# Optimization experiments

Measured on AMD Instinct MI355X. Metric: run time of the kernel, lower is better.

Reference implementation:

```python
import jax, jax.numpy as jnp
import numpy as np

D_MODEL = 1024
NHEAD = 16
HEAD_DIM = D_MODEL // NHEAD
DFF = 4096
EPS = 1e-5


def _layernorm(x, g, b):
    mu = jnp.mean(x, axis=-1, keepdims=True)
    var = jnp.mean(jnp.square(x - mu), axis=-1, keepdims=True)
    return (x - mu) * jax.lax.rsqrt(var + EPS) * g + b


def setup_inputs() -> dict:
    key = jax.random.key(0)
    ks = jax.random.split(key, 20)
    B, S = 2, 2048
    s = 0.02
    inp = {
        "src": jax.random.normal(ks[0], (B, S, D_MODEL), jnp.float32),
        "recompute_idx": jnp.sort(jax.random.randint(ks[1], (409,), 0, S)),
        "cached_k": jax.random.normal(ks[2], (B, NHEAD, S, HEAD_DIM), jnp.float32),
        "cached_v": jax.random.normal(ks[3], (B, NHEAD, S, HEAD_DIM), jnp.float32),
        "Wq": jax.random.normal(ks[4], (D_MODEL, D_MODEL), jnp.float32) * s,
        "bq": jnp.zeros((D_MODEL,), jnp.float32),
        "Wk": jax.random.normal(ks[5], (D_MODEL, D_MODEL), jnp.float32) * s,
        "bk": jnp.zeros((D_MODEL,), jnp.float32),
        "Wv": jax.random.normal(ks[6], (D_MODEL, D_MODEL), jnp.float32) * s,
        "bv": jnp.zeros((D_MODEL,), jnp.float32),
        "Wo": jax.random.normal(ks[7], (D_MODEL, D_MODEL), jnp.float32) * s,
        "bo": jnp.zeros((D_MODEL,), jnp.float32),
        "W1": jax.random.normal(ks[8], (DFF, D_MODEL), jnp.float32) * s,
        "b1": jnp.zeros((DFF,), jnp.float32),
        "W2": jax.random.normal(ks[9], (D_MODEL, DFF), jnp.float32) * s,
        "b2": jnp.zeros((D_MODEL,), jnp.float32),
        "g1": jnp.ones((D_MODEL,), jnp.float32),
        "beta1": jnp.zeros((D_MODEL,), jnp.float32),
        "g2": jnp.ones((D_MODEL,), jnp.float32),
        "beta2": jnp.zeros((D_MODEL,), jnp.float32),
    }
    return inp


def reference(src, recompute_idx, cached_k, cached_v, Wq, bq, Wk, bk, Wv, bv,
              Wo, bo, W1, b1, W2, b2, g1, beta1, g2, beta2):
    B, S, D = src.shape
    H, hd = NHEAD, HEAD_DIM

    # Q for all tokens
    q = (src @ Wq.T + bq).reshape(B, S, H, hd).transpose(0, 2, 1, 3)  # [B,H,S,hd]

    # K/V recomputed only for selected tokens, scattered over cached KV
    src_rec = src[:, recompute_idx, :]  # [B,R,D]
    R = src_rec.shape[1]
    k_rec = (src_rec @ Wk.T + bk).reshape(B, R, H, hd).transpose(0, 2, 1, 3)
    v_rec = (src_rec @ Wv.T + bv).reshape(B, R, H, hd).transpose(0, 2, 1, 3)
    k_full = cached_k.at[:, :, recompute_idx, :].set(k_rec)  # [B,H,S,hd]
    v_full = cached_v.at[:, :, recompute_idx, :].set(v_rec)

    # attention over mixed cached/fresh KV
    scores = jnp.einsum('bhqd,bhkd->bhqk', q, k_full) / np.sqrt(hd).astype(src.dtype)
    probs = jax.nn.softmax(scores, axis=-1)
    attn = jnp.einsum('bhqk,bhkd->bhqd', probs, v_full)
    attn = attn.transpose(0, 2, 1, 3).reshape(B, S, D)
    attn = attn @ Wo.T + bo

    x = _layernorm(src + attn, g1, beta1)
    ff = jax.nn.relu(x @ W1.T + b1) @ W2.T + b2
    x = _layernorm(x + ff, g2, beta2)
    return x
```

## Files before the change

### kernel.cpp

```cpp
#include <hip/hip_runtime.h>
#include <hip/hip_bf16.h>

typedef __attribute__((ext_vector_type(4))) float f32x4;
typedef __attribute__((ext_vector_type(8))) short s16x8;
typedef __attribute__((ext_vector_type(4))) short s16x4;
typedef __attribute__((ext_vector_type(2))) short s16x2;

typedef __attribute__((address_space(1))) const unsigned int guint;
typedef __attribute__((address_space(3))) unsigned int luint;

#define D_MODEL 1024
#define NHEAD 16
#define HEAD_DIM 64
#define DFF 4096
#define SEQ 2048
#define BATCH 2

__device__ __forceinline__ float b2f(short s) {
  union { unsigned int u; float f; } v;
  v.u = ((unsigned int)(unsigned short)s) << 16;
  return v.f;
}
__device__ __forceinline__ short f2b(float f) {
  __hip_bfloat16 h = __float2bfloat16(f);
  return *reinterpret_cast<short*>(&h);
}
__device__ __forceinline__ s16x8 cvt8(f32x4 a, f32x4 b) {
  s16x8 r;
  #pragma unroll
  for (int i = 0; i < 4; ++i) { r[i] = f2b(a[i]); r[i + 4] = f2b(b[i]); }
  return r;
}

template<int MODE, int BN, bool AF32, bool WF32>
__global__ __launch_bounds__(256, 3)
void gemm_nt(const void* __restrict__ Av, const void* __restrict__ Wv,
             const float* __restrict__ bias, short* __restrict__ out,
             int M, int N, int K,
             const int* __restrict__ idx, int R,
             const float* __restrict__ bias2, const float* __restrict__ bias3,
             short* __restrict__ pB, short* __restrict__ pC,
             short* __restrict__ pD)
{
  constexpr bool GLDS = (!AF32 && !WF32);
  constexpr int NI = BN / 32;

  const float* Af = (const float*)Av;
  const short* Ab = (const short*)Av;
  const float* Wf = (const float*)Wv;
  const short* Wb = (const short*)Wv;

  const int tid  = threadIdx.x;
  const int lane = tid & 63, wave = tid >> 6;
  const int g = lane >> 4, l15 = lane & 15;
  const int wm = (wave & 1) * 64, wn = (wave >> 1) * (BN / 2);

  const int nwg = gridDim.x * gridDim.y;
  int lid = blockIdx.y * gridDim.x + blockIdx.x;
  if ((nwg & 7) == 0) lid = (lid & 7) * (nwg >> 3) + (lid >> 3);
  const int bn = lid % gridDim.x;
  const int bm0 = lid / gridDim.x;

  int task = 0, bm = bm0, Mt = M;
  if (MODE == 8) {
    if (bm0 < 32)      { task = 0; bm = bm0;      Mt = M; }
    else if (bm0 < 39) { task = 1; bm = bm0 - 32; Mt = BATCH * R; }
    else               { task = 2; bm = bm0 - 39; Mt = BATCH * R; }
  }

  f32x4 acc[4][NI] = {};

  if constexpr (GLDS) {
    __shared__ short As[2][128][32];
    __shared__ short Bs[2][BN][32];

    const short* Wbase = Wb + ((MODE == 8) ? ((size_t)task << 20) : 0);
    const int nz   = (MODE == 6) ? gridDim.z : 1;
    const int Keff = K / nz;
    const int kOff = (MODE == 6) ? (int)blockIdx.z * Keff : 0;

    const int rA0 = wave * 16 + (lane >> 2);
    const int rA1 = rA0 + 64;
    const int c0  = (lane & 3) * 8;

    auto arow = [&](int r) -> long {
      const int gm = bm * 128 + r;
      const int am = gm < Mt ? gm : Mt - 1;
      if (MODE == 8 && task > 0) {
        const int b0 = am / R;
        return (long)(b0 * SEQ + idx[am - b0 * R]);
      }
      return am;
    };
    const long aR0 = arow(rA0), aR1 = arow(rA1);
    const long wR0 = (long)bn * BN + rA0;

    const short* gA0 = Ab + aR0 * K + kOff + c0;
    const short* gA1 = Ab + aR1 * K + kOff + c0;
    const short* gB0 = Wbase + wR0 * K + kOff + c0;
    const short* gB1 = nullptr;
    if constexpr (BN == 128) gB1 = Wbase + ((long)bn * BN + rA1) * K + kOff + c0;

    auto stage = [&](int buf, int k0) {
      luint* lA0 = (luint*)((short*)As + buf * 4096 + wave * 512);
      luint* lA1 = (luint*)((short*)As + buf * 4096 + (4 + wave) * 512);
      luint* lB0 = (luint*)((short*)Bs + buf * (BN * 32) + wave * 512);
      __builtin_amdgcn_global_load_lds((guint*)(gA0 + k0), lA0, 16, 0, 0);
      __builtin_amdgcn_global_load_lds((guint*)(gA1 + k0), lA1, 16, 0, 0);
      __builtin_amdgcn_global_load_lds((guint*)(gB0 + k0), lB0, 16, 0, 0);
      if constexpr (BN == 128) {
        luint* lB1 = (luint*)((short*)Bs + buf * (BN * 32) + (4 + wave) * 512);
        __builtin_amdgcn_global_load_lds((guint*)(gB1 + k0), lB1, 16, 0, 0);
      }
    };

    stage(0, 0);
    __syncthreads();
    int cur = 0;
    for (int k0 = 0; k0 < Keff; k0 += 32) {
      const int k1 = k0 + 32;
      if (k1 < Keff) stage(cur ^ 1, k1);

      s16x8 af[4], bf4[NI];
      #pragma unroll
      for (int mi = 0; mi < 4; ++mi)
        af[mi] = *(const s16x8*)&As[cur][wm + mi * 16 + l15][g * 8];
      #pragma unroll
      for (int ni = 0; ni < NI; ++ni)
        bf4[ni] = *(const s16x8*)&Bs[cur][wn + ni * 16 + l15][g * 8];
      #pragma unroll
      for (int mi = 0; mi < 4; ++mi)
        #pragma unroll
        for (int ni = 0; ni < NI; ++ni)
          acc[mi][ni] = __builtin_amdgcn_mfma_f32_16x16x32_bf16(af[mi], bf4[ni], acc[mi][ni], 0, 0, 0);

      __syncthreads();
      cur ^= 1;
    }
  } else {
    __shared__ short As[128][40];
    __shared__ short Bs[128][40];
    const int r0 = tid >> 1, c0 = (tid & 1) * 16;
    const int gm0 = bm * 128 + r0;
    const int am0 = gm0 < M ? gm0 : M - 1;
    long aRow0;
    if (MODE == 3 || MODE == 4) {
      const int b0 = am0 / R;
      aRow0 = (long)(b0 * SEQ + idx[am0 - b0 * R]);
    } else {
      aRow0 = am0;
    }
    const long wRow0 = bn * 128 + r0;

    for (int k0 = 0; k0 < K; k0 += 32) {
      __syncthreads();
      if (AF32) {
        f32x4 a0 = *(const f32x4*)(Af + aRow0 * K + k0 + c0);
        f32x4 a1 = *(const f32x4*)(Af + aRow0 * K + k0 + c0 + 4);
        f32x4 a2 = *(const f32x4*)(Af + aRow0 * K + k0 + c0 + 8);
        f32x4 a3 = *(const f32x4*)(Af + aRow0 * K + k0 + c0 + 12);
        *(s16x8*)&As[r0][c0]     = cvt8(a0, a1);
        *(s16x8*)&As[r0][c0 + 8] = cvt8(a2, a3);
      } else {
        *(s16x8*)&As[r0][c0]     = *(const s16x8*)(Ab + aRow0 * K + k0 + c0);
        *(s16x8*)&As[r0][c0 + 8] = *(const s16x8*)(Ab + aRow0 * K + k0 + c0 + 8);
      }
      if (WF32) {
        f32x4 w0 = *(const f32x4*)(Wf + wRow0 * K + k0 + c0);
        f32x4 w1 = *(const f32x4*)(Wf + wRow0 * K + k0 + c0 + 4);
        f32x4 w2 = *(const f32x4*)(Wf + wRow0 * K + k0 + c0 + 8);
        f32x4 w3 = *(const f32x4*)(Wf + wRow0 * K + k0 + c0 + 12);
        *(s16x8*)&Bs[r0][c0]     = cvt8(w0, w1);
        *(s16x8*)&Bs[r0][c0 + 8] = cvt8(w2, w3);
      } else {
        *(s16x8*)&Bs[r0][c0]     = *(const s16x8*)(Wb + wRow0 * K + k0 + c0);
        *(s16x8*)&Bs[r0][c0 + 8] = *(const s16x8*)(Wb + wRow0 * K + k0 + c0 + 8);
      }
      __syncthreads();

      s16x8 af[4], bf4[4];
      #pragma unroll
      for (int mi = 0; mi < 4; ++mi)
        af[mi] = *(const s16x8*)&As[wm + mi * 16 + l15][g * 8];
      #pragma unroll
      for (int ni = 0; ni < 4; ++ni)
        bf4[ni] = *(const s16x8*)&Bs[wn + ni * 16 + l15][g * 8];
      #pragma unroll
      for (int mi = 0; mi < 4; ++mi)
        #pragma unroll
        for (int ni = 0; ni < 4; ++ni)
          acc[mi][ni % NI] = __builtin_amdgcn_mfma_f32_16x16x32_bf16(af[mi], bf4[ni], acc[mi][ni % NI], 0, 0, 0);
    }
  }

  short* outz = out;
  if (MODE == 6) {
    const int z = blockIdx.z;
    outz = (z == 0) ? out : (z == 1) ? pB : (z == 2) ? pC : pD;
  }

  #pragma unroll
  for (int mi = 0; mi < 4; ++mi) {
    #pragma unroll
    for (int ni = 0; ni < NI; ++ni) {
      const int gn = bn * BN + wn + ni * 16 + l15;
      float bv;
      if (MODE == 6)      bv = 0.f;
      else if (MODE == 8) bv = (task == 0) ? bias[gn] : (task == 1) ? bias2[gn] : bias3[gn];
      else                bv = bias[gn];
      #pragma unroll
      for (int r = 0; r < 4; ++r) {
        const int gm = bm * 128 + wm + mi * 16 + g * 4 + r;
        if (MODE == 8) { if (gm >= Mt) continue; }
        else           { if (gm >= M)  continue; }
        float v = acc[mi][ni][r] + bv;
        if (MODE == 1) v = v > 0.f ? v : 0.f;
        if (MODE == 2) v *= 0.125f;
        if (MODE == 0 || MODE == 1) {
          out[(long)gm * N + gn] = f2b(v);
        } else if (MODE == 2) {
          const int b = gm >> 11, s = gm & (SEQ - 1);
          const int h = gn >> 6, d = gn & 63;
          out[(((long)(b * NHEAD + h)) * SEQ + s) * 64 + d] = f2b(v);
        } else if (MODE == 3) {
          const int b = gm / R, s = idx[gm - b * R];
          const int h = gn >> 6, d = gn & 63;
          out[(((long)(b * NHEAD + h)) * SEQ + s) * 64 + d] = f2b(v);
        } else if (MODE == 4) {
          const int b = gm / R, s = idx[gm - b * R];
          const int h = gn >> 6, d = gn & 63;
          out[(((long)(b * NHEAD + h)) * 64 + d) * SEQ + s] = f2b(v);
        } else if (MODE == 6) {
          outz[(long)gm * N + gn] = f2b(v);
        } else {
          const int h = gn >> 6, d = gn & 63;
          if (task == 0) {
            const int b = gm >> 11, s = gm & (SEQ - 1);
            out[(((long)(b * NHEAD + h)) * SEQ + s) * 64 + d] = f2b(v * 0.125f);
          } else if (task == 1) {
            const int b = gm / R, s = idx[gm - b * R];
            (out + (1L << 22))[(((long)(b * NHEAD + h)) * SEQ + s) * 64 + d] = f2b(v);
          } else {
            const int b = gm / R, s = idx[gm - b * R];
            (out + (1L << 23))[(((long)(b * NHEAD + h)) * 64 + d) * SEQ + s] = f2b(v);
          }
        }
      }
    }
  }
}

__global__ __launch_bounds__(256, 2)
void attn_fwd(const short* __restrict__ Q, const short* __restrict__ Kf,
              const short* __restrict__ Vt, short* __restrict__ out)
{
  __shared__ short Kl[2][64][64];
  __shared__ short Vl[2][64][64];

  const int tid  = threadIdx.x;
  const int lane = tid & 63, w = tid >> 6;
  const int g = lane >> 4, l15 = lane & 15;
  const int bh = blockIdx.x;
  const int qt = blockIdx.y;
  const int b  = bh >> 4, h = bh & 15;

  const long base = (long)bh * SEQ * 64;
  const int  q0   = qt * 128 + w * 32;

  s16x8 qf[2][2];
  #pragma unroll
  for (int mi = 0; mi < 2; ++mi)
    #pragma unroll
    for (int c = 0; c < 2; ++c)
      qf[mi][c] = *(const s16x8*)(Q + base + (long)(q0 + mi * 16 + l15) * 64 + c * 32 + g * 8);

  float lsum[2] = {0.f, 0.f};
  f32x4 o[2][4] = {};

  auto ldsw = [](short (*buf)[64], int row, int slot) -> short* {
    return (short*)((char*)&buf[0][0] + row * 128 + ((slot ^ (row & 7)) << 4));
  };

  const int c20 = tid, c21 = tid + 256;
  const int r0 = c20 >> 3, s0 = c20 & 7;
  const int r1 = c21 >> 3, s1 = c21 & 7;

  s16x8 kr[2], vr[2];
  kr[0] = *(const s16x8*)(Kf + base + (long)r0 * 64 + s0 * 8);
  kr[1] = *(const s16x8*)(Kf + base + (long)r1 * 64 + s1 * 8);
  vr[0] = *(const s16x8*)(Vt + base + (long)r0 * SEQ + s0 * 8);
  vr[1] = *(const s16x8*)(Vt + base + (long)r1 * SEQ + s1 * 8);
  *(s16x8*)ldsw(Kl[0], r0, s0) = kr[0];
  *(s16x8*)ldsw(Kl[0], r1, s1) = kr[1];
  *(s16x8*)ldsw(Vl[0], r0, s0) = vr[0];
  *(s16x8*)ldsw(Vl[0], r1, s1) = vr[1];

  int cur = 0;
  for (int t = 0; t < SEQ / 64; ++t) {
    __syncthreads();
    const int kvn = (t + 1) * 64;
    if (kvn < SEQ) {
      kr[0] = *(const s16x8*)(Kf + base + (long)(kvn + r0) * 64 + s0 * 8);
      kr[1] = *(const s16x8*)(Kf + base + (long)(kvn + r1) * 64 + s1 * 8);
      vr[0] = *(const s16x8*)(Vt + base + (long)r0 * SEQ + kvn + s0 * 8);
      vr[1] = *(const s16x8*)(Vt + base + (long)r1 * SEQ + kvn + s1 * 8);
    }

    f32x4 sc[2][4] = {};
    __builtin_amdgcn_s_setprio(1);
    #pragma unroll
    for (int c = 0; c < 2; ++c)
      #pragma unroll
      for (int n = 0; n < 4; ++n) {
        s16x8 kb = *(const s16x8*)ldsw(Kl[cur], n * 16 + l15, c * 4 + g);
        sc[0][n] = __builtin_amdgcn_mfma_f32_16x16x32_bf16(kb, qf[0][c], sc[0][n], 0, 0, 0);
        sc[1][n] = __builtin_amdgcn_mfma_f32_16x16x32_bf16(kb, qf[1][c], sc[1][n], 0, 0, 0);
      }
    __builtin_amdgcn_s_setprio(0);

    s16x8 pa[2][2];
    #pragma unroll
    for (int mi = 0; mi < 2; ++mi) {
      #pragma unroll
      for (int n = 0; n < 4; ++n)
        #pragma unroll
        for (int r = 0; r < 4; ++r) {
          sc[mi][n][r] = __expf(sc[mi][n][r]);
          lsum[mi] += sc[mi][n][r];
        }
      unsigned int wpk[4][2];
      #pragma unroll
      for (int n = 0; n < 4; ++n)
        #pragma unroll
        for (int p = 0; p < 2; ++p)
          asm("v_cvt_pk_bf16_f32 %0, %1, %2"
              : "=v"(wpk[n][p]) : "v"(sc[mi][n][2 * p]), "v"(sc[mi][n][2 * p + 1]));
      #pragma unroll
      for (int c = 0; c < 2; ++c) {
        union { s16x8 v; unsigned int u[4]; } pu;
        #pragma unroll
        for (int p = 0; p < 2; ++p) {
          unsigned int a = wpk[2 * c][p], bb = wpk[2 * c + 1][p];
          asm volatile("v_permlane32_swap_b32 %0, %1" : "+v"(a), "+v"(bb));
          asm volatile("v_permlane16_swap_b32 %0, %1" : "+v"(a), "+v"(bb));
          pu.u[p]     = a;
          pu.u[2 + p] = bb;
        }
        pa[mi][c] = pu.v;
      }
    }

    __builtin_amdgcn_s_setprio(1);
    #pragma unroll
    for (int dt = 0; dt < 4; ++dt)
      #pragma unroll
      for (int c = 0; c < 2; ++c) {
        s16x8 vb = *(const s16x8*)ldsw(Vl[cur], dt * 16 + l15, c * 4 + g);
        o[0][dt] = __builtin_amdgcn_mfma_f32_16x16x32_bf16(pa[0][c], vb, o[0][dt], 0, 0, 0);
        o[1][dt] = __builtin_amdgcn_mfma_f32_16x16x32_bf16(pa[1][c], vb, o[1][dt], 0, 0, 0);
      }
    __builtin_amdgcn_s_setprio(0);

    if (kvn < SEQ) {
      *(s16x8*)ldsw(Kl[cur ^ 1], r0, s0) = kr[0];
      *(s16x8*)ldsw(Kl[cur ^ 1], r1, s1) = kr[1];
      *(s16x8*)ldsw(Vl[cur ^ 1], r0, s0) = vr[0];
      *(s16x8*)ldsw(Vl[cur ^ 1], r1, s1) = vr[1];
    }
    cur ^= 1;
  }

  float inv[2][4];
  #pragma unroll
  for (int mi = 0; mi < 2; ++mi) {
    float tt = lsum[mi];
    tt += __shfl_xor(tt, 16, 64);
    tt += __shfl_xor(tt, 32, 64);
    #pragma unroll
    for (int r = 0; r < 4; ++r)
      inv[mi][r] = 1.0f / __shfl(tt, g * 4 + r, 64);
  }

  #pragma unroll
  for (int mi = 0; mi < 2; ++mi)
    #pragma unroll
    for (int dt = 0; dt < 4; ++dt)
      #pragma unroll
      for (int r = 0; r < 4; ++r) {
        const int q   = q0 + mi * 16 + g * 4 + r;
        const int col = h * 64 + dt * 16 + l15;
        out[((long)(b * SEQ + q)) * D_MODEL + col] = f2b(o[mi][dt][r] * inv[mi][r]);
      }
}

template<bool RES_F32, bool OUT_F32>
__global__ __launch_bounds__(256, 4)
void ln_ff2(const short* __restrict__ p0, const short* __restrict__ p1,
            const float* __restrict__ bias, const void* __restrict__ resv,
            const float* __restrict__ g, const float* __restrict__ beta,
            void* __restrict__ outv)
{
  __shared__ float red[8];
  const int row = blockIdx.x;
  const int tid = threadIdx.x;
  const int lane = tid & 63, w = tid >> 6;

  s16x4 v0 = *(const s16x4*)(p0 + (long)row * D_MODEL + tid * 4);
  s16x4 v1 = *(const s16x4*)(p1 + (long)row * D_MODEL + tid * 4);
  f32x4 vb = *(const f32x4*)(bias + tid * 4);
  float x[4];
  if (RES_F32) {
    f32x4 vr = *(const f32x4*)((const float*)resv + (long)row * D_MODEL + tid * 4);
    #pragma unroll
    for (int i = 0; i < 4; ++i) x[i] = vr[i] + b2f(v0[i]) + b2f(v1[i]) + vb[i];
  } else {
    s16x4 vr = *(const s16x4*)((const short*)resv + (long)row * D_MODEL + tid * 4);
    #pragma unroll
    for (int i = 0; i < 4; ++i) x[i] = b2f(vr[i]) + b2f(v0[i]) + b2f(v1[i]) + vb[i];
  }

  float sum = x[0] + x[1] + x[2] + x[3];
  #pragma unroll
  for (int msk = 32; msk >= 1; msk >>= 1) sum += __shfl_xor(sum, msk, 64);
  if (lane == 0) red[w] = sum;
  __syncthreads();
  sum = red[0] + red[1] + red[2] + red[3];
  const float mu = sum * (1.f / D_MODEL);

  float sq = 0.f;
  #pragma unroll
  for (int i = 0; i < 4; ++i) { float d = x[i] - mu; sq += d * d; }
  #pragma unroll
  for (int msk = 32; msk >= 1; msk >>= 1) sq += __shfl_xor(sq, msk, 64);
  if (lane == 0) red[4 + w] = sq;
  __syncthreads();
  sq = red[4] + red[5] + red[6] + red[7];
  const float rs = rsqrtf(sq * (1.f / D_MODEL) + 1e-5f);

  if (OUT_F32) {
    f32x4 ov;
    #pragma unroll
    for (int i = 0; i < 4; ++i) {
      const int c = tid * 4 + i;
      ov[i] = (x[i] - mu) * rs * g[c] + beta[c];
    }
    *(f32x4*)((float*)outv + (long)row * D_MODEL + tid * 4) = ov;
  } else {
    s16x4 ov;
    #pragma unroll
    for (int i = 0; i < 4; ++i) {
      const int c = tid * 4 + i;
      ov[i] = f2b((x[i] - mu) * rs * g[c] + beta[c]);
    }
    *(s16x4*)((short*)outv + (long)row * D_MODEL + tid * 4) = ov;
  }
}

__global__ __launch_bounds__(256, 4)
void ln_ff4(const short* __restrict__ p0, const short* __restrict__ p1,
            const short* __restrict__ p2, const short* __restrict__ p3,
            const float* __restrict__ bias, const short* __restrict__ xres,
            const float* __restrict__ g, const float* __restrict__ beta,
            float* __restrict__ outv)
{
  __shared__ float red[8];
  const int row = blockIdx.x;
  const int tid = threadIdx.x;
  const int lane = tid & 63, w = tid >> 6;

  s16x4 v0 = *(const s16x4*)(p0 + (long)row * D_MODEL + tid * 4);
  s16x4 v1 = *(const s16x4*)(p1 + (long)row * D_MODEL + tid * 4);
  s16x4 v2 = *(const s16x4*)(p2 + (long)row * D_MODEL + tid * 4);
  s16x4 v3 = *(const s16x4*)(p3 + (long)row * D_MODEL + tid * 4);
  s16x4 vx = *(const s16x4*)(xres + (long)row * D_MODEL + tid * 4);
  f32x4 vb = *(const f32x4*)(bias + tid * 4);
  float x[4];
  #pragma unroll
  for (int i = 0; i < 4; ++i)
    x[i] = b2f(vx[i]) + b2f(v0[i]) + b2f(v1[i]) + b2f(v2[i]) + b2f(v3[i]) + vb[i];

  float sum = x[0] + x[1] + x[2] + x[3];
  #pragma unroll
  for (int msk = 32; msk >= 1; msk >>= 1) sum += __shfl_xor(sum, msk, 64);
  if (lane == 0) red[w] = sum;
  __syncthreads();
  sum = red[0] + red[1] + red[2] + red[3];
  const float mu = sum * (1.f / D_MODEL);

  float sq = 0.f;
  #pragma unroll
  for (int i = 0; i < 4; ++i) { float d = x[i] - mu; sq += d * d; }
  #pragma unroll
  for (int msk = 32; msk >= 1; msk >>= 1) sq += __shfl_xor(sq, msk, 64);
  if (lane == 0) red[4 + w] = sq;
  __syncthreads();
  sq = red[4] + red[5] + red[6] + red[7];
  const float rs = rsqrtf(sq * (1.f / D_MODEL) + 1e-5f);

  f32x4 ov;
  #pragma unroll
  for (int i = 0; i < 4; ++i) {
    const int c = tid * 4 + i;
    ov[i] = (x[i] - mu) * rs * g[c] + beta[c];
  }
  *(f32x4*)(outv + (long)row * D_MODEL + tid * 4) = ov;
}

template<bool RES_F32, bool OUT_F32>
__global__ __launch_bounds__(256, 4)
void ln_res(const short* __restrict__ a, const void* __restrict__ resv,
            const float* __restrict__ g, const float* __restrict__ beta,
            void* __restrict__ outv)
{
  __shared__ float red[8];
  const int row = blockIdx.x;
  const int tid = threadIdx.x;
  const int lane = tid & 63, w = tid >> 6;

  s16x4 va = *(const s16x4*)(a + (long)row * D_MODEL + tid * 4);
  float x[4];
  if (RES_F32) {
    f32x4 vr = *(const f32x4*)((const float*)resv + (long)row * D_MODEL + tid * 4);
    #pragma unroll
    for (int i = 0; i < 4; ++i) x[i] = b2f(va[i]) + vr[i];
  } else {
    s16x4 vr = *(const s16x4*)((const short*)resv + (long)row * D_MODEL + tid * 4);
    #pragma unroll
    for (int i = 0; i < 4; ++i) x[i] = b2f(va[i]) + b2f(vr[i]);
  }
  float sum = x[0] + x[1] + x[2] + x[3];
  #pragma unroll
  for (int msk = 32; msk >= 1; msk >>= 1) sum += __shfl_xor(sum, msk, 64);
  if (lane == 0) red[w] = sum;
  __syncthreads();
  sum = red[0] + red[1] + red[2] + red[3];
  const float mu = sum * (1.f / D_MODEL);

  float sq = 0.f;
  #pragma unroll
  for (int i = 0; i < 4; ++i) { float d = x[i] - mu; sq += d * d; }
  #pragma unroll
  for (int msk = 32; msk >= 1; msk >>= 1) sq += __shfl_xor(sq, msk, 64);
  if (lane == 0) red[4 + w] = sq;
  __syncthreads();
  sq = red[4] + red[5] + red[6] + red[7];
  const float rs = rsqrtf(sq * (1.f / D_MODEL) + 1e-5f);

  if (OUT_F32) {
    f32x4 ov;
    #pragma unroll
    for (int i = 0; i < 4; ++i) {
      const int c = tid * 4 + i;
      ov[i] = (x[i] - mu) * rs * g[c] + beta[c];
    }
    *(f32x4*)((float*)outv + (long)row * D_MODEL + tid * 4) = ov;
  } else {
    s16x4 ov;
    #pragma unroll
    for (int i = 0; i < 4; ++i) {
      const int c = tid * 4 + i;
      ov[i] = f2b((x[i] - mu) * rs * g[c] + beta[c]);
    }
    *(s16x4*)((short*)outv + (long)row * D_MODEL + tid * 4) = ov;
  }
}

__global__ void cvt_all(const float* __restrict__ ck, const float* __restrict__ cv,
                        const float* __restrict__ src,
                        const float* __restrict__ Wq, const float* __restrict__ Wk,
                        const float* __restrict__ Wv, const float* __restrict__ Wo,
                        const float* __restrict__ W1, const float* __restrict__ W2,
                        short* __restrict__ k_ws, short* __restrict__ v_ws,
                        short* __restrict__ srcb,
                        short* __restrict__ Wqb, short* __restrict__ W1b,
                        short* __restrict__ W2b)
{
  for (int i = blockIdx.x * blockDim.x + threadIdx.x; i < 5767168;
       i += gridDim.x * blockDim.x) {
    if (i >= 5242880) {
      const int j = i - 5242880;
      const int bh = j >> 14;
      const int rem = j & 16383;
      const int d = rem & 63;
      const int s0 = (rem >> 6) << 3;
      s16x8 r;
      #pragma unroll
      for (int k = 0; k < 8; ++k)
        r[k] = f2b(cv[((long)bh * SEQ + s0 + k) * 64 + d]);
      *(s16x8*)(v_ws + ((long)bh * 64 + d) * SEQ + s0) = r;
      continue;
    }
    const float* s; short* d; int li;
    if      (i < 1048576) { s = ck;  d = k_ws;           li = i; }
    else if (i < 2097152) { s = src; d = srcb;           li = i - 1048576; }
    else if (i < 2359296) { s = Wq;  d = Wqb;            li = i - 2097152; }
    else if (i < 2621440) { s = Wk;  d = Wqb + 1048576;  li = i - 2359296; }
    else if (i < 2883584) { s = Wv;  d = Wqb + 2097152;  li = i - 2621440; }
    else if (i < 3145728) { s = Wo;  d = Wqb + 3145728;  li = i - 2883584; }
    else if (i < 4194304) { s = W1;  d = W1b;            li = i - 3145728; }
    else                  { s = W2;  d = W2b;            li = i - 4194304; }
    f32x4 v = *(const f32x4*)(s + (long)li * 4);
    s16x4 r;
    #pragma unroll
    for (int j = 0; j < 4; ++j) r[j] = f2b(v[j]);
    *(s16x4*)(d + (long)li * 4) = r;
  }
}

__global__ void cvt_v_t(const float* __restrict__ in, short* __restrict__ out)
{
  const int c2 = blockIdx.x * blockDim.x + threadIdx.x;
  const int bh = c2 >> 14;
  const int rem = c2 & 16383;
  const int d = rem & 63;
  const int s0 = (rem >> 6) << 3;
  s16x8 r;
  #pragma unroll
  for (int j = 0; j < 8; ++j)
    r[j] = f2b(in[((long)bh * SEQ + s0 + j) * 64 + d]);
  *(s16x8*)(out + ((long)bh * 64 + d) * SEQ + s0) = r;
}

__global__ void cvt_f32_bf16(const f32x4* __restrict__ in, s16x4* __restrict__ out, int n4)
{
  for (int i = blockIdx.x * blockDim.x + threadIdx.x; i < n4; i += gridDim.x * blockDim.x) {
    f32x4 v = in[i];
    s16x4 r;
    #pragma unroll
    for (int j = 0; j < 4; ++j) r[j] = f2b(v[j]);
    out[i] = r;
  }
}

extern "C" void kernel_launch(void* const* d_in, const int* in_sizes, int n_in,
                              void* d_out, int out_size, void* d_ws, size_t ws_size,
                              hipStream_t stream)
{
  const float* src = (const float*)d_in[0];
  const int*   idx = (const int*)  d_in[1];
  const float* ck  = (const float*)d_in[2];
  const float* cv  = (const float*)d_in[3];
  const float* Wq  = (const float*)d_in[4];
  const float* bq  = (const float*)d_in[5];
  const float* Wk  = (const float*)d_in[6];
  const float* bk  = (const float*)d_in[7];
  const float* Wv  = (const float*)d_in[8];
  const float* bv  = (const float*)d_in[9];
  const float* Wo  = (const float*)d_in[10];
  const float* bo  = (const float*)d_in[11];
  const float* W1  = (const float*)d_in[12];
  const float* b1  = (const float*)d_in[13];
  const float* W2  = (const float*)d_in[14];
  const float* b2  = (const float*)d_in[15];
  const float* g1  = (const float*)d_in[16];
  const float* be1 = (const float*)d_in[17];
  const float* g2  = (const float*)d_in[18];
  const float* be2 = (const float*)d_in[19];
  float* out = (float*)d_out;

  char* ws = (char*)d_ws;
  const size_t SZ = (size_t)4096 * 1024 * 2;
  short* x_ws    = (short*)(ws);
  short* proj_ws = (short*)(ws + SZ);
  short* q_ws    = (short*)(ws + 2 * SZ);
  short* k_ws    = (short*)(ws + 3 * SZ);
  short* v_ws    = (short*)(ws + 4 * SZ);
  short* attn_ws = (short*)(ws + 5 * SZ);
  short* h_ws    = (short*)(ws + 2 * SZ);
  short* W1b     = (short*)(ws + 6 * SZ);
  short* W2b     = (short*)(ws + 7 * SZ);
  short* srcb    = (short*)(ws + 8 * SZ);
  short* Wqb     = (short*)(ws + 9 * SZ);
  const bool big = ws_size >= 10 * SZ;

  const int M = BATCH * SEQ;
  const int R = 409;
  const int Mr = BATCH * R;
  const int nkv4 = BATCH * NHEAD * SEQ * HEAD_DIM / 4;

  if (big) {
    cvt_all<<<2048, 256, 0, stream>>>(ck, cv, src, Wq, Wk, Wv, Wo, W1, W2,
                                      k_ws, v_ws, srcb, Wqb, W1b, W2b);
    gemm_nt<8, 64, false, false><<<dim3(16, 46), 256, 0, stream>>>(
        srcb, Wqb, bq, q_ws, M, 1024, 1024, idx, R, bk, bv, nullptr, nullptr, nullptr);
    attn_fwd<<<dim3(BATCH * NHEAD, SEQ / 128), 256, 0, stream>>>(q_ws, k_ws, v_ws, attn_ws);
    gemm_nt<6, 64, false, false><<<dim3(16, 32, 2), 256, 0, stream>>>(
        attn_ws, Wqb + 3145728, nullptr, proj_ws, M, 1024, 1024, nullptr, 0,
        nullptr, nullptr, q_ws, nullptr, nullptr);
    ln_ff2<true, false><<<4096, 256, 0, stream>>>(proj_ws, q_ws, bo, src, g1, be1, x_ws);
    gemm_nt<1, 128, false, false><<<dim3(32, 32), 256, 0, stream>>>(
        x_ws, W1b, b1, h_ws, M, DFF, 1024, nullptr, 0, nullptr, nullptr,
        nullptr, nullptr, nullptr);
    gemm_nt<6, 128, false, false><<<dim3(8, 32, 4), 256, 0, stream>>>(
        h_ws, W2b, nullptr, proj_ws, M, 1024, 4096, nullptr, 0,
        nullptr, nullptr, W1b, srcb, Wqb);
    ln_ff4<<<4096, 256, 0, stream>>>(proj_ws, W1b, srcb, Wqb, b2, x_ws, g2, be2, out);
  } else {
    cvt_f32_bf16<<<2048, 256, 0, stream>>>((const f32x4*)ck, (s16x4*)k_ws, nkv4);
    cvt_v_t<<<2048, 256, 0, stream>>>(cv, v_ws);
    gemm_nt<2, 128, true, true><<<dim3(8, 32), 256, 0, stream>>>(
        src, Wq, bq, q_ws, M, 1024, 1024, nullptr, 0, nullptr, nullptr, nullptr, nullptr, nullptr);
    gemm_nt<3, 128, true, true><<<dim3(8, 7), 256, 0, stream>>>(
        src, Wk, bk, k_ws, Mr, 1024, 1024, idx, R, nullptr, nullptr, nullptr, nullptr, nullptr);
    gemm_nt<4, 128, true, true><<<dim3(8, 7), 256, 0, stream>>>(
        src, Wv, bv, v_ws, Mr, 1024, 1024, idx, R, nullptr, nullptr, nullptr, nullptr, nullptr);
    attn_fwd<<<dim3(BATCH * NHEAD, SEQ / 128), 256, 0, stream>>>(q_ws, k_ws, v_ws, attn_ws);
    gemm_nt<0, 128, false, true><<<dim3(8, 32), 256, 0, stream>>>(
        attn_ws, Wo, bo, proj_ws, M, 1024, 1024, nullptr, 0, nullptr, nullptr, nullptr, nullptr, nullptr);
    ln_res<true, false><<<4096, 256, 0, stream>>>(proj_ws, src, g1, be1, x_ws);
    gemm_nt<1, 128, false, true><<<dim3(32, 32), 256, 0, stream>>>(
        x_ws, W1, b1, h_ws, M, DFF, 1024, nullptr, 0, nullptr, nullptr, nullptr, nullptr, nullptr);
    gemm_nt<0, 128, false, true><<<dim3(8, 32), 256, 0, stream>>>(
        h_ws, W2, b2, proj_ws, M, 1024, DFF, nullptr, 0, nullptr, nullptr, nullptr, nullptr, nullptr);
    ln_res<false, true><<<4096, 256, 0, stream>>>(proj_ws, x_ws, g2, be2, out);
  }
}
```

Baseline: 243.1 us.

## Use direct global-to-LDS K/V loads, exp2 softmax, and MFMA row sums in attention

Replaces the register-staged K/V prefetch with global_load_lds async copies into the swizzled LDS buffers, inverting the swizzle on the global side, and moves the barrier to the end of each iteration. The Q scale is folded to include log2(e) so raw v_exp_f32 (exp2) can be used instead of __expf. The per-lane softmax denominator accumulation and final shuffles are replaced by extra MFMAs against a vector of bf16 ones. This cuts VALU and VGPR pressure and frees registers used for staging. The trade-offs are an added MFMA per tile and row sums computed from bf16-rounded probabilities.

```diff
diff --git a/kernel.cpp b/kernel.cpp
--- a/kernel.cpp
+++ b/kernel.cpp
@@ -15,6 +15,7 @@
 #define DFF 4096
 #define SEQ 2048
 #define BATCH 2
+#define QSCALE 0.18033688011112042f
 
 __device__ __forceinline__ float b2f(short s) {
   union { unsigned int u; float f; } v;
@@ -215,7 +216,7 @@
         else           { if (gm >= M)  continue; }
         float v = acc[mi][ni][r] + bv;
         if (MODE == 1) v = v > 0.f ? v : 0.f;
-        if (MODE == 2) v *= 0.125f;
+        if (MODE == 2) v *= QSCALE;
         if (MODE == 0 || MODE == 1) {
           out[(long)gm * N + gn] = f2b(v);
         } else if (MODE == 2) {
@@ -236,7 +237,7 @@
           const int h = gn >> 6, d = gn & 63;
           if (task == 0) {
             const int b = gm >> 11, s = gm & (SEQ - 1);
-            out[(((long)(b * NHEAD + h)) * SEQ + s) * 64 + d] = f2b(v * 0.125f);
+            out[(((long)(b * NHEAD + h)) * SEQ + s) * 64 + d] = f2b(v * QSCALE);
           } else if (task == 1) {
             const int b = gm / R, s = idx[gm - b * R];
             (out + (1L << 22))[(((long)(b * NHEAD + h)) * SEQ + s) * 64 + d] = f2b(v);
@@ -274,37 +275,40 @@
     for (int c = 0; c < 2; ++c)
       qf[mi][c] = *(const s16x8*)(Q + base + (long)(q0 + mi * 16 + l15) * 64 + c * 32 + g * 8);
 
-  float lsum[2] = {0.f, 0.f};
   f32x4 o[2][4] = {};
+  f32x4 os[2] = {};
+
+  s16x8 ones;
+  #pragma unroll
+  for (int j = 0; j < 8; ++j) ones[j] = (short)0x3F80;
 
   auto ldsw = [](short (*buf)[64], int row, int slot) -> short* {
     return (short*)((char*)&buf[0][0] + row * 128 + ((slot ^ (row & 7)) << 4));
   };
 
-  const int c20 = tid, c21 = tid + 256;
-  const int r0 = c20 >> 3, s0 = c20 & 7;
-  const int r1 = c21 >> 3, s1 = c21 & 7;
-
-  s16x8 kr[2], vr[2];
-  kr[0] = *(const s16x8*)(Kf + base + (long)r0 * 64 + s0 * 8);
-  kr[1] = *(const s16x8*)(Kf + base + (long)r1 * 64 + s1 * 8);
-  vr[0] = *(const s16x8*)(Vt + base + (long)r0 * SEQ + s0 * 8);
-  vr[1] = *(const s16x8*)(Vt + base + (long)r1 * SEQ + s1 * 8);
-  *(s16x8*)ldsw(Kl[0], r0, s0) = kr[0];
-  *(s16x8*)ldsw(Kl[0], r1, s1) = kr[1];
-  *(s16x8*)ldsw(Vl[0], r0, s0) = vr[0];
-  *(s16x8*)ldsw(Vl[0], r1, s1) = vr[1];
-
+  const int bo0 = w * 2048 + lane * 16;
+  const int bo1 = bo0 + 1024;
+  const int row0 = bo0 >> 7, ss0 = (((bo0 >> 4) & 7) ^ (row0 & 7));
+  const int row1 = bo1 >> 7, ss1 = (((bo1 >> 4) & 7) ^ (row1 & 7));
+  const short* gK0 = Kf + base + row0 * 64 + ss0 * 8;
+  const short* gK1 = Kf + base + row1 * 64 + ss1 * 8;
+  const short* gV0 = Vt + base + (long)row0 * SEQ + ss0 * 8;
+  const short* gV1 = Vt + base + (long)row1 * SEQ + ss1 * 8;
+
+  auto stage = [&](int buf, int t) {
+    char* kb8 = (char*)&Kl[buf][0][0] + w * 2048;
+    char* vb8 = (char*)&Vl[buf][0][0] + w * 2048;
+    __builtin_amdgcn_global_load_lds((guint*)(gK0 + t * 4096), (luint*)kb8, 16, 0, 0);
+    __builtin_amdgcn_global_load_lds((guint*)(gK1 + t * 4096), (luint*)(kb8 + 1024), 16, 0, 0);
+    __builtin_amdgcn_global_load_lds((guint*)(gV0 + t * 64), (luint*)vb8, 16, 0, 0);
+    __builtin_amdgcn_global_load_lds((guint*)(gV1 + t * 64), (luint*)(vb8 + 1024), 16, 0, 0);
+  };
+
+  stage(0, 0);
+  __syncthreads();
   int cur = 0;
   for (int t = 0; t < SEQ / 64; ++t) {
-    __syncthreads();
-    const int kvn = (t + 1) * 64;
-    if (kvn < SEQ) {
-      kr[0] = *(const s16x8*)(Kf + base + (long)(kvn + r0) * 64 + s0 * 8);
-      kr[1] = *(const s16x8*)(Kf + base + (long)(kvn + r1) * 64 + s1 * 8);
-      vr[0] = *(const s16x8*)(Vt + base + (long)r0 * SEQ + kvn + s0 * 8);
-      vr[1] = *(const s16x8*)(Vt + base + (long)r1 * SEQ + kvn + s1 * 8);
-    }
+    if (t + 1 < SEQ / 64) stage(cur ^ 1, t + 1);
 
     f32x4 sc[2][4] = {};
     __builtin_amdgcn_s_setprio(1);
@@ -325,8 +329,9 @@
       for (int n = 0; n < 4; ++n)
         #pragma unroll
         for (int r = 0; r < 4; ++r) {
-          sc[mi][n][r] = __expf(sc[mi][n][r]);
-          lsum[mi] += sc[mi][n][r];
+          float e;
+          asm("v_exp_f32 %0, %1" : "=v"(e) : "v"(sc[mi][n][r]));
+          sc[mi][n][r] = e;
         }
       unsigned int wpk[4][2];
       #pragma unroll
@@ -359,27 +364,23 @@
         o[0][dt] = __builtin_amdgcn_mfma_f32_16x16x32_bf16(pa[0][c], vb, o[0][dt], 0, 0, 0);
         o[1][dt] = __builtin_amdgcn_mfma_f32_16x16x32_bf16(pa[1][c], vb, o[1][dt], 0, 0, 0);
       }
+    #pragma unroll
+    for (int mi = 0; mi < 2; ++mi)
+      #pragma unroll
+      for (int c = 0; c < 2; ++c)
+        os[mi] = __builtin_amdgcn_mfma_f32_16x16x32_bf16(pa[mi][c], ones, os[mi], 0, 0, 0);
     __builtin_amdgcn_s_setprio(0);
 
-    if (kvn < SEQ) {
-      *(s16x8*)ldsw(Kl[cur ^ 1], r0, s0) = kr[0];
-      *(s16x8*)ldsw(Kl[cur ^ 1], r1, s1) = kr[1];
-      *(s16x8*)ldsw(Vl[cur ^ 1], r0, s0) = vr[0];
-      *(s16x8*)ldsw(Vl[cur ^ 1], r1, s1) = vr[1];
-    }
+    __syncthreads();
     cur ^= 1;
   }
 
   float inv[2][4];
   #pragma unroll
-  for (int mi = 0; mi < 2; ++mi) {
-    float tt = lsum[mi];
-    tt += __shfl_xor(tt, 16, 64);
-    tt += __shfl_xor(tt, 32, 64);
+  for (int mi = 0; mi < 2; ++mi)
     #pragma unroll
     for (int r = 0; r < 4; ++r)
-      inv[mi][r] = 1.0f / __shfl(tt, g * 4 + r, 64);
-  }
+      inv[mi][r] = 1.0f / os[mi][r];
 
   #pragma unroll
   for (int mi = 0; mi < 2; ++mi)
```

Result: faster. 236.9 us (-2.5%).
